# Performance work log

Hardware: AMD Instinct MI355X
Metric: run time of the kernel (lower is better)

The kernel has to match this reference:

```python
import jax, jax.numpy as jnp
import numpy as np

MARGIN = 0.5


def _pairwise_dist(x):
    # Euclidean cdist via ||a||^2 + ||b||^2 - 2ab, with safe sqrt.
    sq = jnp.sum(x * x, axis=-1)  # (N,)
    d2 = sq[:, None] + sq[None, :] - 2.0 * (x @ x.T)
    d2 = jnp.maximum(d2, 0.0)
    return jnp.sqrt(jnp.where(d2 > 0.0, d2, 1.0)) * (d2 > 0.0)


def setup_inputs() -> dict:
    key = jax.random.key(0)
    k1, k2 = jax.random.split(key)
    N, D = 8192, 128
    embeddings = jax.random.normal(k1, (N, D), dtype=jnp.float32)
    labels = jax.random.randint(k2, (N,), 0, 7, dtype=jnp.int64)
    return {"embeddings": embeddings, "labels": labels}


def reference(embeddings, labels):
    N = embeddings.shape[0]
    dist = _pairwise_dist(embeddings)  # (N, N)
    same = labels[:, None] == labels[None, :]
    eye = jnp.eye(N, dtype=bool)
    pos_mask = same & ~eye
    neg_mask = ~same
    big = jnp.asarray(jnp.finfo(dist.dtype).max, dist.dtype)
    # hardest positive: max dist among same-label (excl. self)
    pos_dist = jnp.max(jnp.where(pos_mask, dist, -big), axis=1)
    # hardest negative: min dist among different-label
    neg_dist = jnp.min(jnp.where(neg_mask, dist, big), axis=1)
    valid = jnp.any(pos_mask, axis=1) & jnp.any(neg_mask, axis=1)
    per_row = jax.nn.relu(pos_dist - neg_dist + MARGIN)
    loss_sum = jnp.sum(jnp.where(valid, per_row, 0.0))
    count = jnp.sum(valid)
    return loss_sum / jnp.maximum(count, 1).astype(loss_sum.dtype)
```

## Files before the change

kernel.cpp:

```cpp
#include <hip/hip_runtime.h>

#define N 8192
#define D 128
#define MARGIN 0.5f

typedef __bf16 bf16x8 __attribute__((ext_vector_type(8)));
typedef float f32x4 __attribute__((ext_vector_type(4)));

__device__ __forceinline__ unsigned short f2bf_rne(float f) {
  unsigned u = __float_as_uint(f);
  u += 0x7FFFu + ((u >> 16) & 1u);
  return (unsigned short)(u >> 16);
}

__global__ void k_init(unsigned* __restrict__ posw, unsigned* __restrict__ negw,
                       unsigned* __restrict__ hist, float* __restrict__ acc) {
  int i = blockIdx.x * blockDim.x + threadIdx.x;
  if (i < N) { posw[i] = 0u; negw[i] = 0x7F800000u; }
  if (i < 8) hist[i] = 0u;
  if (i == 0) { acc[0] = 0.f; acc[1] = 0.f; }
}

__global__ void k_convert(const float* __restrict__ x, unsigned short* __restrict__ xb,
                          float* __restrict__ sq) {
  const int row = blockIdx.x;
  const int t = threadIdx.x;
  const float2 v = ((const float2*)x)[row * 64 + t];
  ushort2 o;
  o.x = f2bf_rne(v.x);
  o.y = f2bf_rne(v.y);
  ((ushort2*)xb)[row * 64 + t] = o;
  float s = v.x * v.x + v.y * v.y;
#pragma unroll
  for (int off = 32; off; off >>= 1) s += __shfl_xor(s, off, 64);
  if (t == 0) sq[row] = s;
}

__global__ void k_hist(const int* __restrict__ lab, unsigned* __restrict__ hist) {
  __shared__ unsigned h[8];
  const int t = threadIdx.x;
  if (t < 8) h[t] = 0u;
  __syncthreads();
  const int i = blockIdx.x * blockDim.x + t;
  if (i < N) atomicAdd(&h[lab[i] & 7], 1u);
  __syncthreads();
  if (t < 8) atomicAdd(&hist[t], h[t]);
}

__global__ __launch_bounds__(256, 2) void k_mine(
    const unsigned short* __restrict__ xb, const float* __restrict__ sq,
    const int* __restrict__ lab, unsigned* __restrict__ posw, unsigned* __restrict__ negw) {
  __shared__ __align__(16) unsigned short lds_b[64 * 136];
  __shared__ float lds_sq[64];
  __shared__ int lds_lab[64];

  const int t = threadIdx.x;
  const int w = t >> 6;
  const int lane = t & 63;
  const int col = lane & 15;
  const int quad = lane >> 4;
  const int i0 = blockIdx.x * 128 + w * 32;

  bf16x8 a[2][4];
#pragma unroll
  for (int is = 0; is < 2; ++is) {
    const unsigned short* arow = xb + (size_t)(i0 + is * 16 + col) * D + quad * 8;
#pragma unroll
    for (int k = 0; k < 4; ++k) a[is][k] = *(const bf16x8*)(arow + k * 32);
  }

  float sqi[2][4];
  int labi[2][4], ig[2][4];
#pragma unroll
  for (int is = 0; is < 2; ++is)
#pragma unroll
    for (int r = 0; r < 4; ++r) {
      const int i = i0 + is * 16 + quad * 4 + r;
      ig[is][r] = i;
      sqi[is][r] = sq[i];
      labi[is][r] = lab[i];
    }

  float pos[2][4], neg[2][4];
#pragma unroll
  for (int is = 0; is < 2; ++is)
#pragma unroll
    for (int r = 0; r < 4; ++r) { pos[is][r] = -1.0f; neg[is][r] = 3.402823466e+38f; }

  const int jbase = blockIdx.y * 1024;
  for (int jt = 0; jt < 16; ++jt) {
    const int j0 = jbase + jt * 64;
    __syncthreads();
#pragma unroll
    for (int p = 0; p < 4; ++p) {
      const int row = p * 16 + (t >> 4);
      const int cg = t & 15;
      const uint4 v = *(const uint4*)(xb + (size_t)(j0 + row) * D + cg * 8);
      *(uint4*)(lds_b + row * 136 + cg * 8) = v;
    }
    if (t < 64) {
      lds_sq[t] = sq[j0 + t];
      lds_lab[t] = lab[j0 + t];
    }
    __syncthreads();

#pragma unroll
    for (int s = 0; s < 4; ++s) {
      f32x4 acc0 = {0.f, 0.f, 0.f, 0.f}, acc1 = {0.f, 0.f, 0.f, 0.f};
#pragma unroll
      for (int k = 0; k < 4; ++k) {
        const bf16x8 b = *(const bf16x8*)(lds_b + (s * 16 + col) * 136 + k * 32 + quad * 8);
        acc0 = __builtin_amdgcn_mfma_f32_16x16x32_bf16(a[0][k], b, acc0, 0, 0, 0);
        acc1 = __builtin_amdgcn_mfma_f32_16x16x32_bf16(a[1][k], b, acc1, 0, 0, 0);
      }
      const int jc = s * 16 + col;
      const float sqj = lds_sq[jc];
      const int labj = lds_lab[jc];
      const int jg = j0 + jc;
#pragma unroll
      for (int r = 0; r < 4; ++r) {
        const float d20 = sqi[0][r] + sqj - 2.f * acc0[r];
        const float d21 = sqi[1][r] + sqj - 2.f * acc1[r];
        if (labi[0][r] == labj) {
          if (ig[0][r] != jg) pos[0][r] = fmaxf(pos[0][r], d20);
        } else {
          neg[0][r] = fminf(neg[0][r], d20);
        }
        if (labi[1][r] == labj) {
          if (ig[1][r] != jg) pos[1][r] = fmaxf(pos[1][r], d21);
        } else {
          neg[1][r] = fminf(neg[1][r], d21);
        }
      }
    }
  }

#pragma unroll
  for (int is = 0; is < 2; ++is)
#pragma unroll
    for (int r = 0; r < 4; ++r) {
      float p = pos[is][r], n = neg[is][r];
#pragma unroll
      for (int off = 1; off < 16; off <<= 1) {
        p = fmaxf(p, __shfl_xor(p, off, 64));
        n = fminf(n, __shfl_xor(n, off, 64));
      }
      if (col == 0) {
        atomicMax(posw + ig[is][r], __float_as_uint(fmaxf(p, 0.f)));
        atomicMin(negw + ig[is][r], __float_as_uint(fmaxf(n, 0.f)));
      }
    }
}

__global__ void k_rowloss(const unsigned* __restrict__ posw, const unsigned* __restrict__ negw,
                          const int* __restrict__ lab, const unsigned* __restrict__ hist,
                          float* __restrict__ acc) {
  __shared__ float ls[4], cs[4];
  const int i = blockIdx.x * 256 + threadIdx.x;
  const float pd2 = __uint_as_float(posw[i]);
  const float nd2 = __uint_as_float(negw[i]);
  const unsigned cnt = hist[lab[i] & 7];
  const bool valid = (cnt >= 2u) && (cnt < (unsigned)N);
  float loss = 0.f, c = 0.f;
  if (valid) {
    const float pd = sqrtf(fmaxf(pd2, 0.f));
    const float nd = sqrtf(fmaxf(nd2, 0.f));
    loss = fmaxf(pd - nd + MARGIN, 0.f);
    c = 1.f;
  }
#pragma unroll
  for (int off = 1; off < 64; off <<= 1) {
    loss += __shfl_xor(loss, off, 64);
    c += __shfl_xor(c, off, 64);
  }
  const int wv = threadIdx.x >> 6;
  if ((threadIdx.x & 63) == 0) { ls[wv] = loss; cs[wv] = c; }
  __syncthreads();
  if (threadIdx.x == 0) {
    atomicAdd(acc + 0, ls[0] + ls[1] + ls[2] + ls[3]);
    atomicAdd(acc + 1, cs[0] + cs[1] + cs[2] + cs[3]);
  }
}

__global__ void k_final(const float* __restrict__ acc, float* __restrict__ out) {
  out[0] = acc[0] / fmaxf(acc[1], 1.f);
}

extern "C" void kernel_launch(void* const* d_in, const int* in_sizes, int n_in,
                              void* d_out, int out_size, void* d_ws, size_t ws_size,
                              hipStream_t stream) {
  const float* x = (const float*)d_in[0];
  const int* lab = (const int*)d_in[1];
  char* ws = (char*)d_ws;
  unsigned short* xb = (unsigned short*)ws;
  float* sq = (float*)(ws + (size_t)N * D * 2);
  unsigned* posw = (unsigned*)((char*)sq + (size_t)N * 4);
  unsigned* negw = posw + N;
  unsigned* hist = negw + N;
  float* acc = (float*)(hist + 8);
  float* out = (float*)d_out;

  hipLaunchKernelGGL(k_init, dim3(32), dim3(256), 0, stream, posw, negw, hist, acc);
  hipLaunchKernelGGL(k_convert, dim3(N), dim3(64), 0, stream, x, xb, sq);
  hipLaunchKernelGGL(k_hist, dim3(16), dim3(512), 0, stream, lab, hist);
  hipLaunchKernelGGL(k_mine, dim3(64, 8), dim3(256), 0, stream, xb, sq, lab, posw, negw);
  hipLaunchKernelGGL(k_rowloss, dim3(32), dim3(256), 0, stream, posw, negw, lab, hist, acc);
  hipLaunchKernelGGL(k_final, dim3(1), dim3(1), 0, stream, acc, out);
}
```

Baseline: 113.6 us.

## Fuse prep and tail kernels, swizzle LDS, branchless mining with diagonal fast path

Merges init, convert and histogram into one prep kernel, and folds the final division into the row-loss kernel with a ticket counter. This cuts the launch count from six to three. In the mining kernel the LDS padding is replaced with an XOR swizzle, and the inner mining loop becomes branchless select-based min/max. The self-exclusion check now runs only on diagonal tiles, and sq_i is added once after the reduction. The j-range is also split across twice as many blocks with higher occupancy bounds, which raises the number of atomic updates per row.

New measurement: 107.8 us. -5.1%, faster.

```diff
diff --git a/kernel.cpp b/kernel.cpp
--- a/kernel.cpp
+++ b/kernel.cpp
@@ -3,6 +3,7 @@
 #define N 8192
 #define D 128
 #define MARGIN 0.5f
+#define FLT_BIG 3.402823466e+38f
 
 typedef __bf16 bf16x8 __attribute__((ext_vector_type(8)));
 typedef float f32x4 __attribute__((ext_vector_type(4)));
@@ -13,44 +14,61 @@
   return (unsigned short)(u >> 16);
 }
 
-__global__ void k_init(unsigned* __restrict__ posw, unsigned* __restrict__ negw,
-                       unsigned* __restrict__ hist, float* __restrict__ acc) {
-  int i = blockIdx.x * blockDim.x + threadIdx.x;
-  if (i < N) { posw[i] = 0u; negw[i] = 0x7F800000u; }
-  if (i < 8) hist[i] = 0u;
-  if (i == 0) { acc[0] = 0.f; acc[1] = 0.f; }
-}
-
-__global__ void k_convert(const float* __restrict__ x, unsigned short* __restrict__ xb,
-                          float* __restrict__ sq) {
-  const int row = blockIdx.x;
+__global__ void k_prep(const float* __restrict__ x, const int* __restrict__ lab,
+                       unsigned short* __restrict__ xb, float* __restrict__ sq,
+                       unsigned* __restrict__ posw, unsigned* __restrict__ negw,
+                       unsigned* __restrict__ hist, float* __restrict__ acc,
+                       unsigned* __restrict__ ticket) {
   const int t = threadIdx.x;
-  const float2 v = ((const float2*)x)[row * 64 + t];
-  ushort2 o;
-  o.x = f2bf_rne(v.x);
-  o.y = f2bf_rne(v.y);
-  ((ushort2*)xb)[row * 64 + t] = o;
-  float s = v.x * v.x + v.y * v.y;
-#pragma unroll
-  for (int off = 32; off; off >>= 1) s += __shfl_xor(s, off, 64);
-  if (t == 0) sq[row] = s;
-}
-
-__global__ void k_hist(const int* __restrict__ lab, unsigned* __restrict__ hist) {
-  __shared__ unsigned h[8];
-  const int t = threadIdx.x;
-  if (t < 8) h[t] = 0u;
-  __syncthreads();
-  const int i = blockIdx.x * blockDim.x + t;
-  if (i < N) atomicAdd(&h[lab[i] & 7], 1u);
-  __syncthreads();
-  if (t < 8) atomicAdd(&hist[t], h[t]);
-}
-
-__global__ __launch_bounds__(256, 2) void k_mine(
+  const int row = blockIdx.x * 8 + (t >> 5);
+  const int l32 = t & 31;
+  const float4 v = ((const float4*)x)[row * 32 + l32];
+  ushort4 o;
+  o.x = f2bf_rne(v.x); o.y = f2bf_rne(v.y);
+  o.z = f2bf_rne(v.z); o.w = f2bf_rne(v.w);
+  ((ushort4*)xb)[row * 32 + l32] = o;
+  float s = v.x * v.x + v.y * v.y + v.z * v.z + v.w * v.w;
+#pragma unroll
+  for (int off = 1; off < 32; off <<= 1) s += __shfl_xor(s, off, 64);
+  if (l32 == 0) {
+    sq[row] = s;
+    posw[row] = 0u;
+    negw[row] = 0x7F800000u;
+  }
+
+  if (blockIdx.x == 0) {
+    __shared__ unsigned h[8];
+    if (t < 8) h[t] = 0u;
+    __syncthreads();
+    unsigned long long cA = 0ull, cB = 0ull;
+#pragma unroll
+    for (int it = 0; it < 32; ++it) {
+      const int l = lab[t + it * 256] & 7;
+      if (l < 4) cA += 1ull << (l * 16);
+      else       cB += 1ull << ((l - 4) * 16);
+    }
+#pragma unroll
+    for (int off = 1; off < 64; off <<= 1) {
+      cA += __shfl_xor(cA, off, 64);
+      cB += __shfl_xor(cB, off, 64);
+    }
+    if ((t & 63) == 0) {
+#pragma unroll
+      for (int q = 0; q < 4; ++q) {
+        atomicAdd(&h[q],     (unsigned)((cA >> (q * 16)) & 0xFFFFu));
+        atomicAdd(&h[4 + q], (unsigned)((cB >> (q * 16)) & 0xFFFFu));
+      }
+    }
+    __syncthreads();
+    if (t < 8) hist[t] = h[t];
+    if (t == 0) { acc[0] = 0.f; acc[1] = 0.f; ticket[0] = 0u; }
+  }
+}
+
+__global__ __launch_bounds__(256, 4) void k_mine(
     const unsigned short* __restrict__ xb, const float* __restrict__ sq,
     const int* __restrict__ lab, unsigned* __restrict__ posw, unsigned* __restrict__ negw) {
-  __shared__ __align__(16) unsigned short lds_b[64 * 136];
+  __shared__ __align__(16) unsigned short lds_b[64 * 128];
   __shared__ float lds_sq[64];
   __shared__ int lds_lab[64];
 
@@ -59,7 +77,8 @@
   const int lane = t & 63;
   const int col = lane & 15;
   const int quad = lane >> 4;
-  const int i0 = blockIdx.x * 128 + w * 32;
+  const int iblk = blockIdx.x * 128;
+  const int i0 = iblk + w * 32;
 
   bf16x8 a[2][4];
 #pragma unroll
@@ -69,26 +88,25 @@
     for (int k = 0; k < 4; ++k) a[is][k] = *(const bf16x8*)(arow + k * 32);
   }
 
-  float sqi[2][4];
-  int labi[2][4], ig[2][4];
+  int labi[2][4];
 #pragma unroll
   for (int is = 0; is < 2; ++is)
 #pragma unroll
-    for (int r = 0; r < 4; ++r) {
-      const int i = i0 + is * 16 + quad * 4 + r;
-      ig[is][r] = i;
-      sqi[is][r] = sq[i];
-      labi[is][r] = lab[i];
-    }
+    for (int r = 0; r < 4; ++r) labi[is][r] = lab[i0 + is * 16 + quad * 4 + r];
 
   float pos[2][4], neg[2][4];
 #pragma unroll
   for (int is = 0; is < 2; ++is)
 #pragma unroll
-    for (int r = 0; r < 4; ++r) { pos[is][r] = -1.0f; neg[is][r] = 3.402823466e+38f; }
-
-  const int jbase = blockIdx.y * 1024;
-  for (int jt = 0; jt < 16; ++jt) {
+    for (int r = 0; r < 4; ++r) { pos[is][r] = -FLT_BIG; neg[is][r] = FLT_BIG; }
+
+  const int cm = col & 7;
+  int coff[4];
+#pragma unroll
+  for (int k = 0; k < 4; ++k) coff[k] = col * 256 + (((k * 4 + quad) ^ cm) * 16);
+
+  const int jbase = blockIdx.y * 512;
+  for (int jt = 0; jt < 8; ++jt) {
     const int j0 = jbase + jt * 64;
     __syncthreads();
 #pragma unroll
@@ -96,40 +114,50 @@
       const int row = p * 16 + (t >> 4);
       const int cg = t & 15;
       const uint4 v = *(const uint4*)(xb + (size_t)(j0 + row) * D + cg * 8);
-      *(uint4*)(lds_b + row * 136 + cg * 8) = v;
-    }
-    if (t < 64) {
-      lds_sq[t] = sq[j0 + t];
-      lds_lab[t] = lab[j0 + t];
-    }
-    __syncthreads();
+      *(uint4*)((char*)lds_b + row * 256 + ((cg ^ (row & 7)) * 16)) = v;
+    }
+    if (t < 64) { lds_sq[t] = sq[j0 + t]; lds_lab[t] = lab[j0 + t]; }
+    __syncthreads();
+
+    const bool diag = (j0 < iblk + 128) && (iblk < j0 + 64);
 
 #pragma unroll
     for (int s = 0; s < 4; ++s) {
       f32x4 acc0 = {0.f, 0.f, 0.f, 0.f}, acc1 = {0.f, 0.f, 0.f, 0.f};
 #pragma unroll
       for (int k = 0; k < 4; ++k) {
-        const bf16x8 b = *(const bf16x8*)(lds_b + (s * 16 + col) * 136 + k * 32 + quad * 8);
+        const bf16x8 b = *(const bf16x8*)((const char*)lds_b + s * 4096 + coff[k]);
         acc0 = __builtin_amdgcn_mfma_f32_16x16x32_bf16(a[0][k], b, acc0, 0, 0, 0);
         acc1 = __builtin_amdgcn_mfma_f32_16x16x32_bf16(a[1][k], b, acc1, 0, 0, 0);
       }
       const int jc = s * 16 + col;
       const float sqj = lds_sq[jc];
       const int labj = lds_lab[jc];
-      const int jg = j0 + jc;
-#pragma unroll
-      for (int r = 0; r < 4; ++r) {
-        const float d20 = sqi[0][r] + sqj - 2.f * acc0[r];
-        const float d21 = sqi[1][r] + sqj - 2.f * acc1[r];
-        if (labi[0][r] == labj) {
-          if (ig[0][r] != jg) pos[0][r] = fmaxf(pos[0][r], d20);
-        } else {
-          neg[0][r] = fminf(neg[0][r], d20);
+      if (!diag) {
+#pragma unroll
+        for (int r = 0; r < 4; ++r) {
+          const float m0 = fmaf(-2.f, acc0[r], sqj);
+          const float m1 = fmaf(-2.f, acc1[r], sqj);
+          const bool s0 = (labi[0][r] == labj);
+          const bool s1 = (labi[1][r] == labj);
+          pos[0][r] = fmaxf(pos[0][r], s0 ? m0 : -FLT_BIG);
+          neg[0][r] = fminf(neg[0][r], s0 ? FLT_BIG : m0);
+          pos[1][r] = fmaxf(pos[1][r], s1 ? m1 : -FLT_BIG);
+          neg[1][r] = fminf(neg[1][r], s1 ? FLT_BIG : m1);
         }
-        if (labi[1][r] == labj) {
-          if (ig[1][r] != jg) pos[1][r] = fmaxf(pos[1][r], d21);
-        } else {
-          neg[1][r] = fminf(neg[1][r], d21);
+      } else {
+        const int jg = j0 + jc;
+#pragma unroll
+        for (int r = 0; r < 4; ++r) {
+          const int ir = quad * 4 + r;
+          const float m0 = fmaf(-2.f, acc0[r], sqj);
+          const float m1 = fmaf(-2.f, acc1[r], sqj);
+          const bool s0 = (labi[0][r] == labj) && (jg != i0 + ir);
+          const bool s1 = (labi[1][r] == labj) && (jg != i0 + 16 + ir);
+          pos[0][r] = fmaxf(pos[0][r], s0 ? m0 : -FLT_BIG);
+          neg[0][r] = fminf(neg[0][r], (labi[0][r] == labj) ? FLT_BIG : m0);
+          pos[1][r] = fmaxf(pos[1][r], s1 ? m1 : -FLT_BIG);
+          neg[1][r] = fminf(neg[1][r], (labi[1][r] == labj) ? FLT_BIG : m1);
         }
       }
     }
@@ -146,26 +174,28 @@
         n = fminf(n, __shfl_xor(n, off, 64));
       }
       if (col == 0) {
-        atomicMax(posw + ig[is][r], __float_as_uint(fmaxf(p, 0.f)));
-        atomicMin(negw + ig[is][r], __float_as_uint(fmaxf(n, 0.f)));
-      }
-    }
-}
-
-__global__ void k_rowloss(const unsigned* __restrict__ posw, const unsigned* __restrict__ negw,
-                          const int* __restrict__ lab, const unsigned* __restrict__ hist,
-                          float* __restrict__ acc) {
+        const int i = i0 + is * 16 + quad * 4 + r;
+        const float sqi = sq[i];
+        atomicMax(posw + i, __float_as_uint(fmaxf(sqi + p, 0.f)));
+        atomicMin(negw + i, __float_as_uint(fmaxf(sqi + n, 0.f)));
+      }
+    }
+}
+
+__global__ void k_tail(const unsigned* __restrict__ posw, const unsigned* __restrict__ negw,
+                       const int* __restrict__ lab, const unsigned* __restrict__ hist,
+                       float* __restrict__ acc, unsigned* __restrict__ ticket,
+                       float* __restrict__ out) {
   __shared__ float ls[4], cs[4];
-  const int i = blockIdx.x * 256 + threadIdx.x;
+  const int t = threadIdx.x;
+  const int i = blockIdx.x * 256 + t;
   const float pd2 = __uint_as_float(posw[i]);
   const float nd2 = __uint_as_float(negw[i]);
   const unsigned cnt = hist[lab[i] & 7];
   const bool valid = (cnt >= 2u) && (cnt < (unsigned)N);
   float loss = 0.f, c = 0.f;
   if (valid) {
-    const float pd = sqrtf(fmaxf(pd2, 0.f));
-    const float nd = sqrtf(fmaxf(nd2, 0.f));
-    loss = fmaxf(pd - nd + MARGIN, 0.f);
+    loss = fmaxf(sqrtf(pd2) - sqrtf(fminf(nd2, FLT_BIG)) + MARGIN, 0.f);
     c = 1.f;
   }
 #pragma unroll
@@ -173,17 +203,20 @@
     loss += __shfl_xor(loss, off, 64);
     c += __shfl_xor(c, off, 64);
   }
-  const int wv = threadIdx.x >> 6;
-  if ((threadIdx.x & 63) == 0) { ls[wv] = loss; cs[wv] = c; }
+  const int wv = t >> 6;
+  if ((t & 63) == 0) { ls[wv] = loss; cs[wv] = c; }
   __syncthreads();
-  if (threadIdx.x == 0) {
+  if (t == 0) {
     atomicAdd(acc + 0, ls[0] + ls[1] + ls[2] + ls[3]);
     atomicAdd(acc + 1, cs[0] + cs[1] + cs[2] + cs[3]);
-  }
-}
-
-__global__ void k_final(const float* __restrict__ acc, float* __restrict__ out) {
-  out[0] = acc[0] / fmaxf(acc[1], 1.f);
+    __threadfence();
+    const unsigned tk = atomicAdd(ticket, 1u);
+    if (tk == 31u) {
+      const float lsum = atomicAdd(acc + 0, 0.f);
+      const float csum = atomicAdd(acc + 1, 0.f);
+      out[0] = lsum / fmaxf(csum, 1.f);
+    }
+  }
 }
 
 extern "C" void kernel_launch(void* const* d_in, const int* in_sizes, int n_in,
@@ -197,13 +230,13 @@
   unsigned* posw = (unsigned*)((char*)sq + (size_t)N * 4);
   unsigned* negw = posw + N;
   unsigned* hist = negw + N;
-  float* acc = (float*)(hist + 8);
+  unsigned* ticket = hist + 8;
+  float* acc = (float*)(ticket + 1);
   float* out = (float*)d_out;
 
-  hipLaunchKernelGGL(k_init, dim3(32), dim3(256), 0, stream, posw, negw, hist, acc);
-  hipLaunchKernelGGL(k_convert, dim3(N), dim3(64), 0, stream, x, xb, sq);
-  hipLaunchKernelGGL(k_hist, dim3(16), dim3(512), 0, stream, lab, hist);
-  hipLaunchKernelGGL(k_mine, dim3(64, 8), dim3(256), 0, stream, xb, sq, lab, posw, negw);
-  hipLaunchKernelGGL(k_rowloss, dim3(32), dim3(256), 0, stream, posw, negw, lab, hist, acc);
-  hipLaunchKernelGGL(k_final, dim3(1), dim3(1), 0, stream, acc, out);
-}
+  hipLaunchKernelGGL(k_prep, dim3(1024), dim3(256), 0, stream, x, lab, xb, sq,
+                     posw, negw, hist, acc, ticket);
+  hipLaunchKernelGGL(k_mine, dim3(64, 16), dim3(256), 0, stream, xb, sq, lab, posw, negw);
+  hipLaunchKernelGGL(k_tail, dim3(32), dim3(256), 0, stream, posw, negw, lab, hist,
+                     acc, ticket, out);
+}
```
